# Performance work log

Measured on AMD Instinct MI355X. Metric: run time of the kernel, lower is better.

The kernel has to match this reference:

```python
import jax, jax.numpy as jnp
import numpy as np

ALPHA = 0.0005
BETA = 0.1
MARGIN = 100.0
GCN_WEIGHT = 0.1
EPS = 1e-8


def _bce(pred, tgt):
    # torch.nn.BCELoss with mean reduction (pred already in (0,1))
    return -jnp.mean(tgt * jnp.log(pred) + (1.0 - tgt) * jnp.log(1.0 - pred))


def _gcn_loss(nodes, labels, sample_idx):
    # nodes: [B, M, D], labels: [B, M] in {-1,0,1}, sample_idx: [B, S]
    n2 = jnp.sum(nodes * nodes, axis=-1)                               # [B, M]
    s_nodes = jnp.take_along_axis(nodes, sample_idx[:, :, None], axis=1)  # [B, S, D]
    s_lab = jnp.take_along_axis(labels, sample_idx, axis=1)            # [B, S]
    s2 = jnp.take_along_axis(n2, sample_idx, axis=1)                   # [B, S]
    cross = jnp.einsum('bsd,bmd->bsm', s_nodes, nodes)                 # [B, S, M]
    d2 = jnp.maximum(s2[:, :, None] + n2[:, None, :] - 2.0 * cross, 0.0)
    valid = labels >= 0
    same = (labels[:, None, :] == s_lab[:, :, None]) & valid[:, None, :]
    opp = (labels[:, None, :] != s_lab[:, :, None]) & valid[:, None, :]
    BIG = jnp.float32(1e30)
    # farthest same-label node, closest opposite-label node (L2 distance; sqrt is monotone)
    pos_idx = jnp.argmax(jnp.where(same, d2, -BIG), axis=-1)           # [B, S]
    neg_idx = jnp.argmin(jnp.where(opp, d2, BIG), axis=-1)             # [B, S]
    s_norm = jnp.sqrt(s2)

    def _cos(idx):
        dot = jnp.take_along_axis(cross, idx[:, :, None], axis=2)[..., 0]
        nb = jnp.sqrt(jnp.take_along_axis(n2, idx, axis=1))
        return dot / (jnp.maximum(s_norm, EPS) * jnp.maximum(nb, EPS))

    pos_loss = jnp.where(jnp.any(same, axis=-1), _cos(pos_idx), 0.0)
    neg_loss = jnp.where(jnp.any(opp, axis=-1), _cos(neg_idx), 0.0)
    return jnp.sum(pos_loss + neg_loss)


def setup_inputs() -> dict:
    key = jax.random.key(0)
    ks = jax.random.split(key, 10)
    B, T, D, C, M, S = 32, 750, 2048, 20, 750, 64
    score_act = jax.random.uniform(ks[0], (B, C)) * 0.98 + 0.01   # sigmoid-like probs in (0,1)
    score_bkg = jax.random.uniform(ks[1], (B, C)) * 0.98 + 0.01
    feat_act = jax.random.normal(ks[2], (B, T, D))
    feat_bkg = jax.random.normal(ks[3], (B, T, D))
    label = (jax.random.uniform(ks[4], (B, C)) < 0.3).astype(jnp.float32)
    label = label.at[:, 0].set(1.0)  # guarantee >=1 positive class per video
    gt = jax.random.uniform(ks[5], (B, T, C))
    cas = jax.random.normal(ks[6], (B, T, C))
    nodes = jax.random.normal(ks[7], (B, M, D))
    nodes_label = jax.random.randint(ks[8], (B, M), 0, 2)
    sample_idx = jax.random.randint(ks[9], (B, S), 0, M)
    return {'score_act': score_act, 'score_bkg': score_bkg, 'feat_act': feat_act,
            'feat_bkg': feat_bkg, 'label': label, 'gt': gt, 'cas': cas,
            'nodes': nodes, 'nodes_label': nodes_label, 'sample_idx': sample_idx}


def reference(score_act, score_bkg, feat_act, feat_bkg, label, gt, cas, nodes, nodes_label, sample_idx):
    label_n = label / jnp.sum(label, axis=1, keepdims=True)
    loss_cls = _bce(score_act, label_n)
    label_bkg = jnp.ones_like(label) / label.shape[1]
    loss_be = _bce(score_bkg, label_bkg)
    loss_act = jnp.maximum(MARGIN - jnp.linalg.norm(jnp.mean(feat_act, axis=1), axis=1), 0.0)
    loss_bkg = jnp.linalg.norm(jnp.mean(feat_bkg, axis=1), axis=1)
    loss_um = jnp.mean((loss_act + loss_bkg) ** 2)
    loss_gcn = GCN_WEIGHT * _gcn_loss(nodes, nodes_label, sample_idx)
    return loss_cls + ALPHA * loss_um + BETA * loss_be + loss_gcn
```

## Files before the change

### kernel.cpp

```cpp
#include <hip/hip_runtime.h>
#include <math.h>

#define BB 32
#define TT 750
#define DD 2048
#define CC 20
#define MM 750
#define SS 64
#define MT 64
#define NT 12
#define TSPLIT 8
#define TCH 94

#define GCN_BLOCKS (NT * BB)
#define FEAT_BLOCKS (2 * BB * TSPLIT)
#define TOT_BLOCKS (GCN_BLOCKS + FEAT_BLOCKS + 1)

#define ALPHA_W 0.0005f
#define BETA_W 0.1f
#define MARGIN_W 100.0f
#define GCN_W 0.1f
#define EPS_V 1e-8f

#define WS_LOSS01 0
#define WS_N2ACT 16
#define WS_N2BKG 48
#define WS_GCNB 80
#define WS_S2 128
#define WS_CAND 4096
#define WS_COLSUM 200704

typedef __attribute__((ext_vector_type(8))) short bf16x8;
typedef __attribute__((ext_vector_type(4))) float f32x4;

__device__ __forceinline__ unsigned short f2bf(float f) {
  unsigned int u = __float_as_uint(f);
  return (unsigned short)((u + 0x7FFFu + ((u >> 16) & 1u)) >> 16);
}

__global__ __launch_bounds__(256, 3) void mega_kernel(
    const float* __restrict__ score_act, const float* __restrict__ score_bkg,
    const float* __restrict__ feat_act, const float* __restrict__ feat_bkg,
    const float* __restrict__ label, const float* __restrict__ nodes,
    const int* __restrict__ nlab, const int* __restrict__ sidx,
    float* __restrict__ ws) {
  int bx = blockIdx.x;
  int tid = threadIdx.x;
  int q7 = bx / 7, r7 = bx % 7;

  if (bx < TOT_BLOCKS - 1 && r7 < 3) {
    int idx = q7 * 3 + r7;
    int b = idx / NT, tile = idx % NT;

    __shared__ __align__(16) unsigned short sAh[64 * 64];
    __shared__ __align__(16) unsigned short sBh[64 * 64];
    __shared__ float sS2[SS];
    __shared__ float sN2[MT];
    __shared__ int sSlab[SS];
    __shared__ int sMlab[MT];

    if (tid < SS) {
      sSlab[tid] = nlab[b * MM + sidx[b * SS + tid]];
    } else if (tid < SS + MT) {
      int ml = tid - SS;
      int m = tile * MT + ml;
      sMlab[ml] = (m < MM) ? nlab[b * MM + m] : -2;
    }

    int r = tid >> 2, p = tid & 3;
    const float* aRow = nodes + ((size_t)b * MM + sidx[b * SS + r]) * DD;
    int mrow = tile * MT + r;
    bool bval = (mrow < MM);
    const float* bRow = nodes + ((size_t)b * MM + (bval ? mrow : 0)) * DD;

    int wslot[4];
#pragma unroll
    for (int j = 0; j < 4; ++j) {
      int u = p + 4 * j;
      wslot[j] = r * 64 + ((((u >> 1) ^ (r & 7)) << 1) + (u & 1)) * 4;
    }

    int lane = tid & 63, w = tid >> 6;
    int g = lane >> 4, c = lane & 15;

    float aSq = 0.f, bSq = 0.f;
    f32x4 acc[4];
#pragma unroll
    for (int f = 0; f < 4; ++f) acc[f] = (f32x4){0.f, 0.f, 0.f, 0.f};

    float4 pa[4], pb[4];
#pragma unroll
    for (int j = 0; j < 4; ++j) {
      int off = (p + 4 * j) * 4;
      pa[j] = *(const float4*)(aRow + off);
      pb[j] = *(const float4*)(bRow + off);
    }

    for (int ch = 0; ch < 32; ++ch) {
      __syncthreads();
#pragma unroll
      for (int j = 0; j < 4; ++j) {
        float4 v = pa[j];
        aSq += v.x * v.x + v.y * v.y + v.z * v.z + v.w * v.w;
        unsigned int lo = (unsigned int)f2bf(v.x) | ((unsigned int)f2bf(v.y) << 16);
        unsigned int hi = (unsigned int)f2bf(v.z) | ((unsigned int)f2bf(v.w) << 16);
        *(uint2*)&sAh[wslot[j]] = make_uint2(lo, hi);
        float4 t = pb[j];
        bSq += t.x * t.x + t.y * t.y + t.z * t.z + t.w * t.w;
        lo = (unsigned int)f2bf(t.x) | ((unsigned int)f2bf(t.y) << 16);
        hi = (unsigned int)f2bf(t.z) | ((unsigned int)f2bf(t.w) << 16);
        *(uint2*)&sBh[wslot[j]] = make_uint2(lo, hi);
      }
      __syncthreads();
      if (ch < 31) {
        const float* ap = aRow + (ch + 1) * 64;
        const float* bp = bRow + (ch + 1) * 64;
#pragma unroll
        for (int j = 0; j < 4; ++j) {
          int off = (p + 4 * j) * 4;
          pa[j] = *(const float4*)(ap + off);
          pb[j] = *(const float4*)(bp + off);
        }
      }
#pragma unroll
      for (int kk = 0; kk < 2; ++kk) {
        int su = kk * 4 + g;
        int arow = w * 16 + c;
        bf16x8 af = *(const bf16x8*)&sAh[arow * 64 + (su ^ (arow & 7)) * 8];
#pragma unroll
        for (int f = 0; f < 4; ++f) {
          int brow = f * 16 + c;
          bf16x8 bfr = *(const bf16x8*)&sBh[brow * 64 + (su ^ (brow & 7)) * 8];
          acc[f] = __builtin_amdgcn_mfma_f32_16x16x32_bf16(af, bfr, acc[f], 0, 0, 0);
        }
      }
    }

    aSq += __shfl_down(aSq, 2, 4);
    aSq += __shfl_down(aSq, 1, 4);
    bSq += __shfl_down(bSq, 2, 4);
    bSq += __shfl_down(bSq, 1, 4);
    if (p == 0) {
      sS2[r] = aSq;
      sN2[r] = bSq;
    }
    __syncthreads();

    if (tile == 0 && tid < SS) ws[WS_S2 + b * SS + tid] = sS2[tid];

#pragma unroll
    for (int reg = 0; reg < 4; ++reg) {
      int s = w * 16 + g * 4 + reg;
      int slab = sSlab[s];
      float s2v = sS2[s];
      float posD = -3.4e38f, posC = 0.f, posN = 0.f;
      int posI = -1;
      float negD = 3.4e38f, negC = 0.f, negN = 0.f;
      int negI = -1;
#pragma unroll
      for (int f = 0; f < 4; ++f) {
        int ml = f * 16 + c;
        int lab = sMlab[ml];
        float cv = acc[f][reg];
        float n2 = sN2[ml];
        float d2 = fmaxf(s2v + n2 - 2.f * cv, 0.f);
        if (lab >= 0 && lab == slab && (posI < 0 || d2 > posD)) {
          posD = d2; posI = tile * MT + ml; posC = cv; posN = n2;
        }
        if (lab >= 0 && lab != slab && (negI < 0 || d2 < negD)) {
          negD = d2; negI = tile * MT + ml; negC = cv; negN = n2;
        }
      }
#pragma unroll
      for (int off = 8; off; off >>= 1) {
        float oD = __shfl_down(posD, off, 16);
        int oI = __shfl_down(posI, off, 16);
        float oC = __shfl_down(posC, off, 16);
        float oN = __shfl_down(posN, off, 16);
        bool take = (oI >= 0) &&
                    (posI < 0 || oD > posD || (oD == posD && oI < posI));
        if (take) { posD = oD; posI = oI; posC = oC; posN = oN; }
        oD = __shfl_down(negD, off, 16);
        oI = __shfl_down(negI, off, 16);
        oC = __shfl_down(negC, off, 16);
        oN = __shfl_down(negN, off, 16);
        take = (oI >= 0) &&
               (negI < 0 || oD < negD || (oD == negD && oI < negI));
        if (take) { negD = oD; negI = oI; negC = oC; negN = oN; }
      }
      if (c == 0) {
        size_t base = (((size_t)b * SS + s) * NT + tile) * 8;
        *(float4*)&ws[WS_CAND + base] =
            make_float4(posD, __int_as_float(posI), posC, posN);
        *(float4*)&ws[WS_CAND + base + 4] =
            make_float4(negD, __int_as_float(negI), negC, negN);
      }
    }
  } else if (bx < TOT_BLOCKS - 1) {
    int idx = q7 * 4 + (r7 - 3);
    int tz = idx >> 8;
    int rem = idx & 255;
    int fb = rem >> 3;
    int blk = rem & 7;
    const float* feat = tz ? feat_bkg : feat_act;
    int t0 = blk * TCH;
    int t1 = t0 + TCH < TT ? t0 + TCH : TT;
    const float* bp = feat + (size_t)fb * TT * DD + tid * 4;
    f32x4 a00 = {0.f, 0.f, 0.f, 0.f}, a01 = {0.f, 0.f, 0.f, 0.f};
    f32x4 a10 = {0.f, 0.f, 0.f, 0.f}, a11 = {0.f, 0.f, 0.f, 0.f};
    f32x4 a20 = {0.f, 0.f, 0.f, 0.f}, a21 = {0.f, 0.f, 0.f, 0.f};
    f32x4 a30 = {0.f, 0.f, 0.f, 0.f}, a31 = {0.f, 0.f, 0.f, 0.f};
    int t = t0;
    for (; t + 3 < t1; t += 4) {
      const f32x4* p0 = (const f32x4*)(bp + (size_t)t * DD);
      const f32x4* p1 = (const f32x4*)(bp + (size_t)(t + 1) * DD);
      const f32x4* p2 = (const f32x4*)(bp + (size_t)(t + 2) * DD);
      const f32x4* p3 = (const f32x4*)(bp + (size_t)(t + 3) * DD);
      f32x4 v00 = __builtin_nontemporal_load(p0);
      f32x4 v01 = __builtin_nontemporal_load(p0 + 256);
      f32x4 v10 = __builtin_nontemporal_load(p1);
      f32x4 v11 = __builtin_nontemporal_load(p1 + 256);
      f32x4 v20 = __builtin_nontemporal_load(p2);
      f32x4 v21 = __builtin_nontemporal_load(p2 + 256);
      f32x4 v30 = __builtin_nontemporal_load(p3);
      f32x4 v31 = __builtin_nontemporal_load(p3 + 256);
      a00 += v00; a01 += v01;
      a10 += v10; a11 += v11;
      a20 += v20; a21 += v21;
      a30 += v30; a31 += v31;
    }
    for (; t < t1; ++t) {
      const f32x4* p0 = (const f32x4*)(bp + (size_t)t * DD);
      a00 += __builtin_nontemporal_load(p0);
      a01 += __builtin_nontemporal_load(p0 + 256);
    }
    f32x4 r0 = (a00 + a10) + (a20 + a30);
    f32x4 r1 = (a01 + a11) + (a21 + a31);
    float* cs = ws + WS_COLSUM +
                ((size_t)(tz * BB + fb) * TSPLIT + blk) * DD + tid * 4;
    *(f32x4*)cs = r0;
    *(f32x4*)(cs + 1024) = r1;
  } else {
    float vc = 0.f, vb = 0.f;
    for (int i = tid; i < BB * CC; i += 256) {
      int b = i / CC, c = i % CC;
      float rs = 0.f;
      for (int k = 0; k < CC; ++k) rs += label[b * CC + k];
      float ln = label[b * CC + c] / rs;
      float pa = score_act[i];
      vc += ln * logf(pa) + (1.f - ln) * logf(1.f - pa);
      float pb = score_bkg[i];
      const float tb = 1.f / (float)CC;
      vb += tb * logf(pb) + (1.f - tb) * logf(1.f - pb);
    }
    for (int off = 32; off; off >>= 1) {
      vc += __shfl_down(vc, off, 64);
      vb += __shfl_down(vb, off, 64);
    }
    __shared__ float rc[4], rb[4];
    if ((tid & 63) == 0) {
      rc[tid >> 6] = vc;
      rb[tid >> 6] = vb;
    }
    __syncthreads();
    if (tid == 0) {
      ws[WS_LOSS01] = -(rc[0] + rc[1] + rc[2] + rc[3]) / (float)(BB * CC);
      ws[WS_LOSS01 + 1] = -(rb[0] + rb[1] + rb[2] + rb[3]) / (float)(BB * CC);
    }
  }
}

__global__ __launch_bounds__(256) void tail_kernel(float* __restrict__ ws) {
  int bx = blockIdx.x, tid = threadIdx.x;
  if (bx < 64) {
    int tz = bx >> 5, fb = bx & 31;
    const float* cs = ws + WS_COLSUM + (size_t)(tz * BB + fb) * TSPLIT * DD;
    int d0 = tid * 8;
    float4 A0 = make_float4(0.f, 0.f, 0.f, 0.f);
    float4 A1 = make_float4(0.f, 0.f, 0.f, 0.f);
    for (int blk = 0; blk < TSPLIT; ++blk) {
      const float* pp = cs + blk * DD + d0;
      float4 u = *(const float4*)pp;
      float4 v = *(const float4*)(pp + 4);
      A0.x += u.x; A0.y += u.y; A0.z += u.z; A0.w += u.w;
      A1.x += v.x; A1.y += v.y; A1.z += v.z; A1.w += v.w;
    }
    const float inv = 1.f / (float)TT;
    float m0 = A0.x * inv, m1 = A0.y * inv, m2 = A0.z * inv, m3 = A0.w * inv;
    float m4 = A1.x * inv, m5 = A1.y * inv, m6 = A1.z * inv, m7 = A1.w * inv;
    float v = m0 * m0 + m1 * m1 + m2 * m2 + m3 * m3 +
              m4 * m4 + m5 * m5 + m6 * m6 + m7 * m7;
    for (int off = 32; off; off >>= 1) v += __shfl_down(v, off, 64);
    __shared__ float red[4];
    if ((tid & 63) == 0) red[tid >> 6] = v;
    __syncthreads();
    if (tid == 0)
      ws[(tz ? WS_N2BKG : WS_N2ACT) + fb] = red[0] + red[1] + red[2] + red[3];
  } else {
    int b = bx - 64;
    if (tid < SS) {
      const float* cb = ws + WS_CAND + ((size_t)b * SS + tid) * NT * 8;
      float posD = -3.4e38f, posC = 0.f, posN = 0.f;
      int posI = -1;
      float negD = 3.4e38f, negC = 0.f, negN = 0.f;
      int negI = -1;
      for (int t = 0; t < NT; ++t) {
        float4 pq = *(const float4*)&cb[t * 8];
        int oI = __float_as_int(pq.y);
        if (oI >= 0 && (posI < 0 || pq.x > posD || (pq.x == posD && oI < posI))) {
          posD = pq.x; posI = oI; posC = pq.z; posN = pq.w;
        }
        float4 qq = *(const float4*)&cb[t * 8 + 4];
        oI = __float_as_int(qq.y);
        if (oI >= 0 && (negI < 0 || qq.x < negD || (qq.x == negD && oI < negI))) {
          negD = qq.x; negI = oI; negC = qq.z; negN = qq.w;
        }
      }
      float snorm = sqrtf(ws[WS_S2 + b * SS + tid]);
      float sden = fmaxf(snorm, EPS_V);
      float pl = (posI >= 0) ? posC / (sden * fmaxf(sqrtf(posN), EPS_V)) : 0.f;
      float nl = (negI >= 0) ? negC / (sden * fmaxf(sqrtf(negN), EPS_V)) : 0.f;
      float v = pl + nl;
      for (int off = 32; off; off >>= 1) v += __shfl_down(v, off, 64);
      if (tid == 0) ws[WS_GCNB + b] = v;
    }
  }
}

__global__ void final_kernel(const float* __restrict__ ws,
                             float* __restrict__ out) {
  int tid = threadIdx.x;
  float um = 0.f, g = 0.f;
  if (tid < BB) {
    float la = fmaxf(MARGIN_W - sqrtf(ws[WS_N2ACT + tid]), 0.f);
    float lb = sqrtf(ws[WS_N2BKG + tid]);
    um = (la + lb) * (la + lb);
    g = ws[WS_GCNB + tid];
  }
  for (int off = 32; off; off >>= 1) {
    um += __shfl_down(um, off, 64);
    g += __shfl_down(g, off, 64);
  }
  if (tid == 0)
    out[0] = ws[WS_LOSS01] + BETA_W * ws[WS_LOSS01 + 1] +
             ALPHA_W * (um / (float)BB) + GCN_W * g;
}

extern "C" void kernel_launch(void* const* d_in, const int* in_sizes, int n_in,
                              void* d_out, int out_size, void* d_ws,
                              size_t ws_size, hipStream_t stream) {
  const float* score_act = (const float*)d_in[0];
  const float* score_bkg = (const float*)d_in[1];
  const float* feat_act = (const float*)d_in[2];
  const float* feat_bkg = (const float*)d_in[3];
  const float* label = (const float*)d_in[4];
  const float* nodes = (const float*)d_in[7];
  const int* nlab = (const int*)d_in[8];
  const int* sidx = (const int*)d_in[9];
  float* out = (float*)d_out;
  float* wsf = (float*)d_ws;

  mega_kernel<<<TOT_BLOCKS, 256, 0, stream>>>(
      score_act, score_bkg, feat_act, feat_bkg, label, nodes, nlab, sidx, wsf);
  tail_kernel<<<96, 256, 0, stream>>>(wsf);
  final_kernel<<<1, 64, 0, stream>>>(wsf, out);
}
```

Measured before the change: 123.8 us.

## Use atomic work-stealing queue for feature column-sum units across all blocks

Replaces the statically assigned feature-reduction blocks with a dynamic work queue. Every block, including the GCN and BCE blocks once they finish their own work, pulls finer-grained 47-row chunks through a global atomic counter. The aim is to balance the memory-bound feature streaming against the compute-heavy GCN tiles and cut tail imbalance. The cost is an extra memset launch, atomic traffic and two block syncs per unit, plus twice as many partial sums for the tail kernel to reduce.

Result: slower. 136.2 us (+10.0%).

```diff
diff --git a/kernel.cpp b/kernel.cpp
--- a/kernel.cpp
+++ b/kernel.cpp
@@ -9,12 +9,13 @@
 #define SS 64
 #define MT 64
 #define NT 12
-#define TSPLIT 8
-#define TCH 94
+#define FSPLIT 16
+#define FROWS 47
+#define FUNITS (2 * BB * FSPLIT)
 
 #define GCN_BLOCKS (NT * BB)
-#define FEAT_BLOCKS (2 * BB * TSPLIT)
-#define TOT_BLOCKS (GCN_BLOCKS + FEAT_BLOCKS + 1)
+#define IDLE_BLOCKS 512
+#define TOT_BLOCKS (GCN_BLOCKS + IDLE_BLOCKS + 1)
 
 #define ALPHA_W 0.0005f
 #define BETA_W 0.1f
@@ -26,6 +27,7 @@
 #define WS_N2ACT 16
 #define WS_N2BKG 48
 #define WS_GCNB 80
+#define WS_CNT 112
 #define WS_S2 128
 #define WS_CAND 4096
 #define WS_COLSUM 200704
@@ -196,15 +198,49 @@
             make_float4(negD, __int_as_float(negI), negC, negN);
       }
     }
-  } else if (bx < TOT_BLOCKS - 1) {
-    int idx = q7 * 4 + (r7 - 3);
-    int tz = idx >> 8;
-    int rem = idx & 255;
-    int fb = rem >> 3;
-    int blk = rem & 7;
+  } else if (bx == TOT_BLOCKS - 1) {
+    float vc = 0.f, vb = 0.f;
+    for (int i = tid; i < BB * CC; i += 256) {
+      int b = i / CC, c = i % CC;
+      float rs = 0.f;
+      for (int k = 0; k < CC; ++k) rs += label[b * CC + k];
+      float ln = label[b * CC + c] / rs;
+      float pa = score_act[i];
+      vc += ln * logf(pa) + (1.f - ln) * logf(1.f - pa);
+      float pb = score_bkg[i];
+      const float tb = 1.f / (float)CC;
+      vb += tb * logf(pb) + (1.f - tb) * logf(1.f - pb);
+    }
+    for (int off = 32; off; off >>= 1) {
+      vc += __shfl_down(vc, off, 64);
+      vb += __shfl_down(vb, off, 64);
+    }
+    __shared__ float rc[4], rb[4];
+    if ((tid & 63) == 0) {
+      rc[tid >> 6] = vc;
+      rb[tid >> 6] = vb;
+    }
+    __syncthreads();
+    if (tid == 0) {
+      ws[WS_LOSS01] = -(rc[0] + rc[1] + rc[2] + rc[3]) / (float)(BB * CC);
+      ws[WS_LOSS01 + 1] = -(rb[0] + rb[1] + rb[2] + rb[3]) / (float)(BB * CC);
+    }
+  }
+
+  __shared__ int sUnit;
+  for (;;) {
+    if (tid == 0) sUnit = atomicAdd((int*)(ws + WS_CNT), 1);
+    __syncthreads();
+    int u = sUnit;
+    __syncthreads();
+    if (u >= FUNITS) break;
+    int tz = u >> 9;
+    int rem = u & 511;
+    int fb = rem >> 4;
+    int sub = rem & 15;
     const float* feat = tz ? feat_bkg : feat_act;
-    int t0 = blk * TCH;
-    int t1 = t0 + TCH < TT ? t0 + TCH : TT;
+    int t0 = sub * FROWS;
+    int t1 = t0 + FROWS < TT ? t0 + FROWS : TT;
     const float* bp = feat + (size_t)fb * TT * DD + tid * 4;
     f32x4 a00 = {0.f, 0.f, 0.f, 0.f}, a01 = {0.f, 0.f, 0.f, 0.f};
     f32x4 a10 = {0.f, 0.f, 0.f, 0.f}, a11 = {0.f, 0.f, 0.f, 0.f};
@@ -237,36 +273,9 @@
     f32x4 r0 = (a00 + a10) + (a20 + a30);
     f32x4 r1 = (a01 + a11) + (a21 + a31);
     float* cs = ws + WS_COLSUM +
-                ((size_t)(tz * BB + fb) * TSPLIT + blk) * DD + tid * 4;
+                ((size_t)(tz * BB + fb) * FSPLIT + sub) * DD + tid * 4;
     *(f32x4*)cs = r0;
     *(f32x4*)(cs + 1024) = r1;
-  } else {
-    float vc = 0.f, vb = 0.f;
-    for (int i = tid; i < BB * CC; i += 256) {
-      int b = i / CC, c = i % CC;
-      float rs = 0.f;
-      for (int k = 0; k < CC; ++k) rs += label[b * CC + k];
-      float ln = label[b * CC + c] / rs;
-      float pa = score_act[i];
-      vc += ln * logf(pa) + (1.f - ln) * logf(1.f - pa);
-      float pb = score_bkg[i];
-      const float tb = 1.f / (float)CC;
-      vb += tb * logf(pb) + (1.f - tb) * logf(1.f - pb);
-    }
-    for (int off = 32; off; off >>= 1) {
-      vc += __shfl_down(vc, off, 64);
-      vb += __shfl_down(vb, off, 64);
-    }
-    __shared__ float rc[4], rb[4];
-    if ((tid & 63) == 0) {
-      rc[tid >> 6] = vc;
-      rb[tid >> 6] = vb;
-    }
-    __syncthreads();
-    if (tid == 0) {
-      ws[WS_LOSS01] = -(rc[0] + rc[1] + rc[2] + rc[3]) / (float)(BB * CC);
-      ws[WS_LOSS01 + 1] = -(rb[0] + rb[1] + rb[2] + rb[3]) / (float)(BB * CC);
-    }
   }
 }
 
@@ -274,11 +283,11 @@
   int bx = blockIdx.x, tid = threadIdx.x;
   if (bx < 64) {
     int tz = bx >> 5, fb = bx & 31;
-    const float* cs = ws + WS_COLSUM + (size_t)(tz * BB + fb) * TSPLIT * DD;
+    const float* cs = ws + WS_COLSUM + (size_t)(tz * BB + fb) * FSPLIT * DD;
     int d0 = tid * 8;
     float4 A0 = make_float4(0.f, 0.f, 0.f, 0.f);
     float4 A1 = make_float4(0.f, 0.f, 0.f, 0.f);
-    for (int blk = 0; blk < TSPLIT; ++blk) {
+    for (int blk = 0; blk < FSPLIT; ++blk) {
       const float* pp = cs + blk * DD + d0;
       float4 u = *(const float4*)pp;
       float4 v = *(const float4*)(pp + 4);
@@ -360,6 +369,8 @@
   float* out = (float*)d_out;
   float* wsf = (float*)d_ws;
 
+  hipMemsetAsync((char*)d_ws + WS_CNT * sizeof(float), 0, sizeof(int), stream);
+
   mega_kernel<<<TOT_BLOCKS, 256, 0, stream>>>(
       score_act, score_bkg, feat_act, feat_bkg, label, nodes, nlab, sidx, wsf);
   tail_kernel<<<96, 256, 0, stream>>>(wsf);
```
